# Kernel tuning notes

Measured on AMD Instinct MI355X. Metric: run time of the kernel, lower is better.

Reference implementation:

```python
import jax, jax.numpy as jnp
import numpy as np

C = 32
SHIFTS = (1, 2, 4)
KSIZE = 4  # trans_layer: kernel KSIZE+1, stride KSIZE, pad KSIZE//2
EPS_NORM = 1e-12
EPS_BN = 1e-5


def _make_diff_kernels(c):
    # 8 fixed 3x3 difference kernels, tiled per channel for depthwise conv.
    d1 = np.array([[[-1, 0, 0], [0, 1, 0], [0, 0, 0]],
                   [[0, -1, 0], [0, 1, 0], [0, 0, 0]],
                   [[0, 0, -1], [0, 1, 0], [0, 0, 0]],
                   [[0, 0, 0], [0, 1, -1], [0, 0, 0]]], dtype=np.float32)
    d1 = d1.reshape(4, 1, 3, 3)
    d2 = d1[:, :, ::-1, ::-1].copy()
    delta = np.concatenate([d1, d2], axis=0)          # [8,1,3,3]
    return jnp.asarray(np.tile(delta, (c, 1, 1, 1)))  # [8C,1,3,3]


DIFF_KERNELS = _make_diff_kernels(C)


def conv2d(x, w, stride=1, pad=0, dilation=1, groups=1):
    return jax.lax.conv_general_dilated(
        x, w, (stride, stride), [(pad, pad), (pad, pad)],
        rhs_dilation=(dilation, dilation),
        dimension_numbers=('NCHW', 'OIHW', 'NCHW'),
        feature_group_count=groups)


def l2norm(x, axis=-1):
    n = jnp.sqrt(jnp.sum(x * x, axis=axis, keepdims=True))
    return x / jnp.maximum(n, EPS_NORM)


def setup_inputs() -> dict:
    key = jax.random.key(0)
    ks = jax.random.split(key, 8)
    S = len(SHIFTS)
    return {
        'cen': jax.random.normal(ks[0], (2, C, 256, 256), jnp.float32),
        'trans_W': jax.random.normal(ks[1], (C, C, 5, 5), jnp.float32) * 0.05,
        'trans_b': jax.random.normal(ks[2], (C,), jnp.float32) * 0.05,
        'query_W': jax.random.normal(ks[3], (C, C, 1, 1), jnp.float32) * 0.05,
        'value_W': jax.random.normal(ks[4], (S, C, C, 1, 1), jnp.float32) * 0.05,
        'key_W': jax.random.normal(ks[5], (S, C, C, 1, 1), jnp.float32) * 0.05,
        'out_W': jax.random.normal(ks[6], (C, C, 1, 1), jnp.float32) * 0.05,
        'bn_gamma': jnp.ones((C,), jnp.float32),
        'bn_beta': jnp.zeros((C,), jnp.float32),
        'bn_mean': jnp.zeros((C,), jnp.float32),
        'bn_var': jnp.ones((C,), jnp.float32),
    }


def reference(cen, trans_W, trans_b, query_W, value_W, key_W, out_W,
              bn_gamma, bn_beta, bn_mean, bn_var):
    b, _, w, h = cen.shape
    S = len(SHIFTS)
    size = (w * h) // (KSIZE * KSIZE)

    # trans_layer: kernel KSIZE+1, stride KSIZE, pad KSIZE//2
    kv_cen = conv2d(cen, trans_W, stride=KSIZE, pad=KSIZE // 2) \
        + trans_b[None, :, None, None]

    keys, values = [], []
    for i, d in enumerate(SHIFTS):
        v = conv2d(cen, value_W[i])          # [b,C,w,h]
        k = conv2d(kv_cen, key_W[i])         # [b,C,w',h']
        # depthwise dilated difference conv -> 8 outputs per channel
        v = conv2d(v, DIFF_KERNELS, pad=d, dilation=d, groups=C)  # [b,8C,w,h]
        k = conv2d(k, DIFF_KERNELS, pad=d, dilation=d, groups=C)  # [b,8C,w',h']
        keys.append(k)
        values.append(v)

    querys = conv2d(kv_cen, query_W)  # [b,C,w',h']

    keys = jnp.stack(keys, axis=2).reshape(b, C, 8 * S, size)       # [b,C,8S,size]
    values = jnp.stack(values, axis=2).reshape(b, C, 8 * S, w * h)  # [b,C,8S,wh]

    keys = jnp.swapaxes(l2norm(keys, -1), -2, -1)        # [b,C,size,8S]
    querys = l2norm(querys.reshape(b, C, 1, size), -1)   # [b,C,1,size]

    score = jnp.matmul(querys, keys)   # [b,C,1,8S]  cosine sims
    score = l2norm(score, -1)
    out = jnp.matmul(score, values).reshape(b, C, w, h)

    # out_conv: 1x1 conv -> BN (eval mode, running stats) -> ReLU
    out = conv2d(out, out_W)
    inv = jax.lax.rsqrt(bn_var + EPS_BN)
    out = (out - bn_mean[None, :, None, None]) * (bn_gamma * inv)[None, :, None, None] \
        + bn_beta[None, :, None, None]
    return jax.nn.relu(out)
```

## Files before the change

kernel.cpp:

```cpp
#include <hip/hip_runtime.h>
#include <hip/hip_bf16.h>


#define CC 32
#define HW 256
#define KVW 64

__global__ __launch_bounds__(256, 2) void k1_trans(const float* __restrict__ cen,
                                                   const float* __restrict__ tW,
                                                   const float* __restrict__ tB,
                                                   float* __restrict__ kv) {
  int bid = blockIdx.x;
  int b = bid >> 8, cog = (bid >> 6) & 3, y = bid & 63;
  int tid = threadIdx.x;
  int x = tid & 63;
  int w = __builtin_amdgcn_readfirstlane(tid >> 6);
  int co0 = cog * 8 + w * 2;

  float acc0 = 0.f, acc1 = 0.f;
  const float4 z4 = {0.f, 0.f, 0.f, 0.f};

  int roff[5];
  bool rok[5];
#pragma unroll
  for (int r = 0; r < 5; r++) {
    int row = 4 * y - 2 + r;
    rok[r] = (row >= 0);
    roff[r] = (row < 0 ? 0 : row) * HW;
  }

  for (int ci = 0; ci < CC; ci += 4) {
    const float* pc[4];
#pragma unroll
    for (int c = 0; c < 4; c++) pc[c] = cen + (size_t)(b * CC + ci + c) * 65536 + 4 * x;
    float4 A[4][5], B[4][5];
#pragma unroll
    for (int c = 0; c < 4; c++) {
#pragma unroll
      for (int r = 0; r < 5; r++) {
        A[c][r] = (x > 0) ? *(const float4*)(pc[c] + roff[r] - 4) : z4;
        B[c][r] = *(const float4*)(pc[c] + roff[r]);
      }
    }
#pragma unroll
    for (int r = 0; r < 5; r++) {
      if (!rok[r]) continue;
#pragma unroll
      for (int c = 0; c < 4; c++) {
        const float* wa = tW + (co0 * CC + ci + c) * 25 + r * 5;
        const float* wb = wa + CC * 25;
        acc0 += wa[0] * A[c][r].z + wa[1] * A[c][r].w + wa[2] * B[c][r].x +
                wa[3] * B[c][r].y + wa[4] * B[c][r].z;
        acc1 += wb[0] * A[c][r].z + wb[1] * A[c][r].w + wb[2] * B[c][r].x +
                wb[3] * B[c][r].y + wb[4] * B[c][r].z;
      }
    }
  }
  kv[((b * CC + co0) * KVW + y) * KVW + x] = acc0 + tB[co0];
  kv[((b * CC + co0 + 1) * KVW + y) * KVW + x] = acc1 + tB[co0 + 1];
}

__device__ inline float wred64(float v) {
#pragma unroll
  for (int off = 1; off < 64; off <<= 1) v += __shfl_xor(v, off);
  return v;
}

__global__ __launch_bounds__(1024) void k2_scores(const float* __restrict__ kv,
                                                  const float* __restrict__ qW,
                                                  const float* __restrict__ kW,
                                                  float* __restrict__ scores) {
  __shared__ alignas(16) float kl[3][4096];
  __shared__ float wred[16][52];
  __shared__ float srl[24];
  int bc = blockIdx.x;
  int b = bc >> 5, c = bc & 31;
  int tid = threadIdx.x;
  int lane = tid & 63, w = tid >> 6;
  int xx = tid & 63;
  int ybase = tid >> 6;

  float qreg[4];
#pragma unroll
  for (int r = 0; r < 4; r++) {
    int px = r * 1024 + tid;
    float q = 0.f, k0 = 0.f, k1 = 0.f, k2 = 0.f;
    for (int ci = 0; ci < CC; ci++) {
      float val = kv[(b * CC + ci) * 4096 + px];
      q += qW[c * CC + ci] * val;
      k0 += kW[(0 * CC + c) * CC + ci] * val;
      k1 += kW[(1 * CC + c) * CC + ci] * val;
      k2 += kW[(2 * CC + c) * CC + ci] * val;
    }
    qreg[r] = q;
    kl[0][px] = k0;
    kl[1][px] = k1;
    kl[2][px] = k2;
  }
  __syncthreads();

  float q2 = 0.f;
#pragma unroll
  for (int r = 0; r < 4; r++) q2 += qreg[r] * qreg[r];
  q2 = wred64(q2);
  if (lane == 0) wred[w][48] = q2;

  constexpr int DYt[8] = {-1, -1, -1, 0, 1, 1, 1, 0};
  constexpr int DXt[8] = {-1, 0, 1, 1, 1, 0, -1, -1};
#pragma unroll
  for (int j = 0; j < 24; j++) {
    const int i = j >> 3, n = j & 7, d = 1 << i;
    const int dy = DYt[n], dx = DXt[n];
    int xn = xx + dx * d;
    bool xok = (xn >= 0 && xn < KVW);
    float dacc = 0.f, macc = 0.f;
#pragma unroll
    for (int r = 0; r < 4; r++) {
      int yy = r * 16 + ybase;
      int px = yy * KVW + xx;
      float kc = kl[i][px];
      int yn = yy + dy * d;
      float kn = (xok && yn >= 0 && yn < KVW) ? kl[i][yn * KVW + xn] : 0.f;
      float df = kc - kn;
      dacc += qreg[r] * df;
      macc += df * df;
    }
    dacc = wred64(dacc);
    macc = wred64(macc);
    if (lane == 0) {
      wred[w][j] = dacc;
      wred[w][24 + j] = macc;
    }
  }
  __syncthreads();
  if (tid < 24) {
    float D = 0.f, M = 0.f, Q2 = 0.f;
    for (int w2 = 0; w2 < 16; w2++) {
      D += wred[w2][tid];
      M += wred[w2][24 + tid];
      Q2 += wred[w2][48];
    }
    float sr = D / (fmaxf(sqrtf(M), 1e-12f) * fmaxf(sqrtf(Q2), 1e-12f));
    srl[tid] = sr;
  }
  __syncthreads();
  if (tid < 24) {
    float r2 = 0.f;
    for (int j = 0; j < 24; j++) r2 += srl[j] * srl[j];
    float s = srl[tid] / fmaxf(sqrtf(r2), 1e-12f);
    scores[(b * CC + c) * 24 + tid] = s;
  }
}

__global__ __launch_bounds__(256) void k3a_values(const float* __restrict__ cen,
                                                  const float* __restrict__ vW,
                                                  __hip_bfloat16* __restrict__ v) {
  int bid = blockIdx.x;
  int b = bid >> 10, blk = bid & 1023;
  int tid = threadIdx.x;
  int lane = tid & 63;
  int cg = __builtin_amdgcn_readfirstlane(tid >> 6);
  int px = blk * 64 + lane;

  float cr[CC];
#pragma unroll
  for (int ci = 0; ci < CC; ci++) cr[ci] = cen[(b * CC + ci) * 65536 + px];

#pragma unroll
  for (int i = 0; i < 3; i++) {
#pragma unroll
    for (int cc = 0; cc < 8; cc++) {
      int c = cg * 8 + cc;
      const float* wp = vW + (i * CC + c) * CC;
      float a = 0.f;
#pragma unroll
      for (int ci = 0; ci < CC; ci++) a += wp[ci] * cr[ci];
      v[((i * 2 + b) * CC + c) * 65536 + px] = __float2bfloat16(a);
    }
  }
}

__global__ __launch_bounds__(256) void k3b_combine(const __hip_bfloat16* __restrict__ v,
                                                   const float* __restrict__ scores,
                                                   const float* __restrict__ oW,
                                                   const float* __restrict__ gamma,
                                                   const float* __restrict__ beta,
                                                   const float* __restrict__ mean,
                                                   const float* __restrict__ var,
                                                   float* __restrict__ out) {
  __shared__ alignas(16) float vt[3 * 24 * 24 * 4];
  __shared__ alignas(16) float sl[27][32];
  __shared__ alignas(16) float owl[32][32];
  __shared__ float bns[32], bnb[32];

  int bid = blockIdx.x;
  int b = bid >> 8, tile = bid & 255;
  int ty = tile >> 4, tx = tile & 15;
  int tid = threadIdx.x;
  int ly = tid >> 4, lx = tid & 15;

  for (int f = tid; f < 24 * 32; f += 256) {
    int j = f >> 5, c = f & 31;
    sl[j][c] = scores[(b * CC + c) * 24 + j];
  }
  for (int f = tid; f < 1024; f += 256) owl[f >> 5][f & 31] = oW[f];
  if (tid < 32) {
    float inv = rsqrtf(var[tid] + 1e-5f);
    float sc = gamma[tid] * inv;
    bns[tid] = sc;
    bnb[tid] = beta[tid] - mean[tid] * sc;
  }
  __syncthreads();
  if (tid < 32) {
#pragma unroll
    for (int i = 0; i < 3; i++) {
      float s = 0.f;
      for (int n = 0; n < 8; n++) s += sl[i * 8 + n][tid];
      sl[24 + i][tid] = s;
    }
  }

  int ldsoff[4], pxoff[4], ibase[4];
  bool okp[4];
#pragma unroll
  for (int it = 0; it < 4; it++) {
    int p = tid + it * 256;
    bool act = (p < 864);
    int pp = act ? p : 0;
    int i = pp / 288;
    int rem = pp - i * 288;
    int r = rem / 12;
    int col = (rem - r * 12) * 2;
    int gy = ty * 16 + r - 4, gx = tx * 16 + col - 4;
    okp[it] = act && gy >= 0 && gy < HW && gx >= 0 && gx < HW;
    pxoff[it] = gy * HW + gx;
    ibase[it] = (i * 2 + b) * CC;
    ldsoff[it] = ((i * 24 + r) * 24 + col) * 4;
  }

  constexpr int DYt[8] = {-1, -1, -1, 0, 1, 1, 1, 0};
  constexpr int DXt[8] = {-1, 0, 1, 1, 1, 0, -1, -1};

  float acc[32];
#pragma unroll
  for (int co = 0; co < 32; co++) acc[co] = 0.f;

  unsigned int pf[4][4];
  const unsigned short* vs = (const unsigned short*)v;

#pragma unroll
  for (int it = 0; it < 4; it++)
#pragma unroll
    for (int cp = 0; cp < 4; cp++)
      pf[it][cp] = okp[it]
                       ? *(const unsigned int*)(vs + (((size_t)(ibase[it] + cp)) << 16) +
                                                pxoff[it])
                       : 0u;

  for (int cg = 0; cg < 8; cg++) {
    __syncthreads();
#pragma unroll
    for (int it = 0; it < 4; it++) {
      if (it == 3 && tid >= 96) continue;
      float4 lo, hi;
      lo.x = __uint_as_float(pf[it][0] << 16);
      lo.y = __uint_as_float(pf[it][1] << 16);
      lo.z = __uint_as_float(pf[it][2] << 16);
      lo.w = __uint_as_float(pf[it][3] << 16);
      hi.x = __uint_as_float(pf[it][0] & 0xffff0000u);
      hi.y = __uint_as_float(pf[it][1] & 0xffff0000u);
      hi.z = __uint_as_float(pf[it][2] & 0xffff0000u);
      hi.w = __uint_as_float(pf[it][3] & 0xffff0000u);
      *(float4*)&vt[ldsoff[it]] = lo;
      *(float4*)&vt[ldsoff[it] + 4] = hi;
    }
    if (cg < 7) {
      int cb = (cg + 1) * 4;
#pragma unroll
      for (int it = 0; it < 4; it++)
#pragma unroll
        for (int cp = 0; cp < 4; cp++)
          pf[it][cp] = okp[it] ? *(const unsigned int*)(vs +
                                                        (((size_t)(ibase[it] + cb + cp))
                                                         << 16) +
                                                        pxoff[it])
                               : 0u;
    }
    __syncthreads();

    float4 pre = {0.f, 0.f, 0.f, 0.f};
#pragma unroll
    for (int i = 0; i < 3; i++) {
      const int d = 1 << i;
      float4 S4 = *(const float4*)&sl[24 + i][cg * 4];
      float4 ctr = *(const float4*)&vt[((i * 24 + (ly + 4)) * 24 + (lx + 4)) * 4];
      pre.x += S4.x * ctr.x;
      pre.y += S4.y * ctr.y;
      pre.z += S4.z * ctr.z;
      pre.w += S4.w * ctr.w;
#pragma unroll
      for (int n = 0; n < 8; n++) {
        float4 sj = *(const float4*)&sl[i * 8 + n][cg * 4];
        float4 nb = *(const float4*)&vt[((i * 24 + (ly + 4 + DYt[n] * d)) * 24 +
                                         (lx + 4 + DXt[n] * d)) * 4];
        pre.x -= sj.x * nb.x;
        pre.y -= sj.y * nb.y;
        pre.z -= sj.z * nb.z;
        pre.w -= sj.w * nb.w;
      }
    }
#pragma unroll
    for (int co = 0; co < 32; co++) {
      float4 ow = *(const float4*)&owl[co][cg * 4];
      acc[co] += ow.x * pre.x + ow.y * pre.y + ow.z * pre.z + ow.w * pre.w;
    }
  }

  int gy = ty * 16 + ly, gx = tx * 16 + lx;
#pragma unroll
  for (int co = 0; co < 32; co++) {
    float val = acc[co] * bns[co] + bnb[co];
    out[((size_t)(b * CC + co) << 16) + gy * HW + gx] = fmaxf(val, 0.f);
  }
}

extern "C" void kernel_launch(void* const* d_in, const int* in_sizes, int n_in,
                              void* d_out, int out_size, void* d_ws, size_t ws_size,
                              hipStream_t stream) {
  const float* cen = (const float*)d_in[0];
  const float* trans_W = (const float*)d_in[1];
  const float* trans_b = (const float*)d_in[2];
  const float* query_W = (const float*)d_in[3];
  const float* value_W = (const float*)d_in[4];
  const float* key_W = (const float*)d_in[5];
  const float* out_W = (const float*)d_in[6];
  const float* bn_gamma = (const float*)d_in[7];
  const float* bn_beta = (const float*)d_in[8];
  const float* bn_mean = (const float*)d_in[9];
  const float* bn_var = (const float*)d_in[10];
  float* out = (float*)d_out;

  float* kv = (float*)d_ws;
  float* scores = (float*)((char*)d_ws + 524288);
  __hip_bfloat16* v = (__hip_bfloat16*)((char*)d_ws + 524288 + 8192);

  k1_trans<<<512, 256, 0, stream>>>(cen, trans_W, trans_b, kv);
  k2_scores<<<64, 1024, 0, stream>>>(kv, query_W, key_W, scores);
  k3a_values<<<2048, 256, 0, stream>>>(cen, value_W, v);
  k3b_combine<<<512, 256, 0, stream>>>(v, scores, out_W, bn_gamma, bn_beta, bn_mean,
                                       bn_var, out);
}
```

Measured before the change: 187.3 us.

## Split score kernel: precompute query/key 1x1 maps in separate parallel kernel

```diff
diff --git a/kernel.cpp b/kernel.cpp
--- a/kernel.cpp
+++ b/kernel.cpp
@@ -60,16 +60,50 @@
   kv[((b * CC + co0 + 1) * KVW + y) * KVW + x] = acc1 + tB[co0 + 1];
 }
 
+__global__ __launch_bounds__(256) void k2m_maps(const float* __restrict__ kv,
+                                                const float* __restrict__ qW,
+                                                const float* __restrict__ kW,
+                                                float* __restrict__ qmap,
+                                                float* __restrict__ kmap) {
+  int bid = blockIdx.x;
+  int b = bid >> 6, chunk = bid & 63;
+  int tid = threadIdx.x;
+  int lane = tid & 63;
+  int cg = __builtin_amdgcn_readfirstlane(tid >> 6);
+  int px = chunk * 64 + lane;
+
+  float cr[CC];
+#pragma unroll
+  for (int ci = 0; ci < CC; ci++) cr[ci] = kv[(b * CC + ci) * 4096 + px];
+
+#pragma unroll
+  for (int cc = 0; cc < 8; cc++) {
+    int c = cg * 8 + cc;
+    const float* qp = qW + c * CC;
+    float q = 0.f;
+#pragma unroll
+    for (int ci = 0; ci < CC; ci++) q += qp[ci] * cr[ci];
+    qmap[(b * CC + c) * 4096 + px] = q;
+#pragma unroll
+    for (int i = 0; i < 3; i++) {
+      const float* kp = kW + (i * CC + c) * CC;
+      float k = 0.f;
+#pragma unroll
+      for (int ci = 0; ci < CC; ci++) k += kp[ci] * cr[ci];
+      kmap[((i * 2 + b) * CC + c) * 4096 + px] = k;
+    }
+  }
+}
+
 __device__ inline float wred64(float v) {
 #pragma unroll
   for (int off = 1; off < 64; off <<= 1) v += __shfl_xor(v, off);
   return v;
 }
 
-__global__ __launch_bounds__(1024) void k2_scores(const float* __restrict__ kv,
-                                                  const float* __restrict__ qW,
-                                                  const float* __restrict__ kW,
-                                                  float* __restrict__ scores) {
+__global__ __launch_bounds__(1024) void k2r_scores(const float* __restrict__ qmap,
+                                                   const float* __restrict__ kmap,
+                                                   float* __restrict__ scores) {
   __shared__ alignas(16) float kl[3][4096];
   __shared__ float wred[16][52];
   __shared__ float srl[24];
@@ -82,20 +116,12 @@
 
   float qreg[4];
 #pragma unroll
-  for (int r = 0; r < 4; r++) {
-    int px = r * 1024 + tid;
-    float q = 0.f, k0 = 0.f, k1 = 0.f, k2 = 0.f;
-    for (int ci = 0; ci < CC; ci++) {
-      float val = kv[(b * CC + ci) * 4096 + px];
-      q += qW[c * CC + ci] * val;
-      k0 += kW[(0 * CC + c) * CC + ci] * val;
-      k1 += kW[(1 * CC + c) * CC + ci] * val;
-      k2 += kW[(2 * CC + c) * CC + ci] * val;
-    }
-    qreg[r] = q;
-    kl[0][px] = k0;
-    kl[1][px] = k1;
-    kl[2][px] = k2;
+  for (int r = 0; r < 4; r++)
+    qreg[r] = qmap[(b * CC + c) * 4096 + r * 1024 + tid];
+  for (int f = tid; f < 3072; f += 1024) {
+    int i = f >> 10, p4 = (f & 1023) << 2;
+    *(float4*)&kl[i][p4] =
+        *(const float4*)(kmap + ((size_t)((i * 2 + b) * CC + c) << 12) + p4);
   }
   __syncthreads();
 
@@ -342,10 +368,13 @@
 
   float* kv = (float*)d_ws;
   float* scores = (float*)((char*)d_ws + 524288);
-  __hip_bfloat16* v = (__hip_bfloat16*)((char*)d_ws + 524288 + 8192);
+  __hip_bfloat16* v = (__hip_bfloat16*)((char*)d_ws + 532480);
+  float* qmap = (float*)((char*)d_ws + 21504000);
+  float* kmap = (float*)((char*)d_ws + 22552576);
 
   k1_trans<<<512, 256, 0, stream>>>(cen, trans_W, trans_b, kv);
-  k2_scores<<<64, 1024, 0, stream>>>(kv, query_W, key_W, scores);
+  k2m_maps<<<128, 256, 0, stream>>>(kv, query_W, key_W, qmap, kmap);
+  k2r_scores<<<64, 1024, 0, stream>>>(qmap, kmap, scores);
   k3a_values<<<2048, 256, 0, stream>>>(cen, value_W, v);
   k3b_combine<<<512, 256, 0, stream>>>(v, scores, out_W, bn_gamma, bn_beta, bn_mean,
                                        bn_var, out);
```

Result: slower. 197.5 us (+5.5%).
